# Kernel tuning notes

Measured on AMD Instinct MI355X. Metric: run time of the kernel, lower is better.

## Reference

```python
import jax, jax.numpy as jnp
import numpy as np

L, EMB, H, K, TASKS = 4, 256, 4, 3, 128
ATOM_VOCAB, BOND_VOCAB = 100, 10
N_NODES, N_EDGES, N_GRAPHS = 50000, 800000, 1024
FC_IN = EMB * (K + H + 1)  # 2048


def setup_inputs() -> dict:
    key = jax.random.key(0)
    ks = jax.random.split(key, 16)
    x = jax.random.randint(ks[0], (N_NODES, 9), 0, ATOM_VOCAB)
    edge_index = jax.random.randint(ks[1], (2, N_EDGES), 0, N_NODES)
    edge_attr = jax.random.randint(ks[2], (N_EDGES, 3), 0, BOND_VOCAB)
    batch = jnp.sort(jax.random.randint(ks[3], (N_NODES,), 0, N_GRAPHS))
    g = lambda k, shape, scale: jax.random.normal(k, shape, jnp.float32) * scale
    return {
        'x': x, 'edge_index': edge_index, 'edge_attr': edge_attr, 'batch': batch,
        'atom_emb': g(ks[4], (9, ATOM_VOCAB, EMB), 0.1),
        'bond_emb': g(ks[5], (L, 3, BOND_VOCAB, EMB), 0.1),
        'Wq_w': g(ks[6], (L, EMB, H * EMB), EMB ** -0.5),
        'Wq_b': jnp.zeros((L, H * EMB), jnp.float32),
        'Wk_w': g(ks[7], (L, EMB, H * EMB), EMB ** -0.5),
        'Wk_b': jnp.zeros((L, H * EMB), jnp.float32),
        'fc_w': g(ks[8], (L, FC_IN, EMB), FC_IN ** -0.5),
        'fc_b': jnp.zeros((L, EMB), jnp.float32),
        'ln_g': jnp.ones((L, EMB), jnp.float32),
        'ln_b': jnp.zeros((L, EMB), jnp.float32),
        'out_w': g(ks[9], (EMB, TASKS), EMB ** -0.5),
        'out_b': jnp.zeros((TASKS,), jnp.float32),
    }


def _layernorm(h, g, b, eps=1e-5):
    mu = h.mean(-1, keepdims=True)
    var = ((h - mu) ** 2).mean(-1, keepdims=True)
    return (h - mu) * jax.lax.rsqrt(var + eps) * g + b


def _linear_attn(h, wq, bq, wk, bk):
    # simple kernel, non-blockwise path of full_attention_conv
    N = h.shape[0]
    q = (h @ wq + bq).reshape(N, H, EMB)
    k = (h @ wk + bk).reshape(N, H, EMB)
    q = q / jnp.linalg.norm(q, axis=2, keepdims=True)
    k = k / jnp.linalg.norm(k, axis=2, keepdims=True)
    # value = x broadcast over heads -> contract with x directly
    kvs = jnp.einsum('lhm,ld->hmd', k, h)                 # [H,M,D]
    num = jnp.einsum('nhm,hmd->nhd', q, kvs) + h.sum(0)[None, None, :]
    ks_sum = k.sum(0)                                      # [H,M]
    denom = jnp.einsum('nhm,hm->nh', q, ks_sum)[..., None] + jnp.float32(N)
    return (num / denom).reshape(N, H * EMB)


def _gnn_high_order(h, row, col, e_emb):
    N = h.shape[0]
    ones = jnp.ones(row.shape[0], jnp.float32)
    deg_i = jax.ops.segment_sum(ones, row, num_segments=N)
    deg_j = jax.ops.segment_sum(ones, col, num_segments=N)
    dinv_i = jnp.where(deg_i > 0, deg_i ** -0.5, 0.0)
    dinv_j = jnp.where(deg_j > 0, deg_j ** -0.5, 0.0)
    adj_val = (dinv_i[row] * dinv_j[col])[:, None]         # [E,1]
    message = jax.ops.segment_sum(adj_val * e_emb, row, num_segments=N)
    xs = [h]
    for _ in range(K):
        spmm = jax.ops.segment_sum(adj_val * xs[-1][col], row, num_segments=N)
        xs.append(spmm + message)
    return jnp.concatenate(xs, axis=1)                     # [N, (K+1)*EMB]


def reference(x, edge_index, edge_attr, batch, atom_emb, bond_emb, Wq_w, Wq_b,
              Wk_w, Wk_b, fc_w, fc_b, ln_g, ln_b, out_w, out_b):
    row, col = edge_index[0], edge_index[1]
    # AtomEncoder: sum of 9 per-feature embeddings
    h = sum(atom_emb[f][x[:, f]] for f in range(9))        # [N, EMB]
    for i in range(L):
        x1 = _linear_attn(h, Wq_w[i], Wq_b[i], Wk_w[i], Wk_b[i])
        e_emb = sum(bond_emb[i, f][edge_attr[:, f]] for f in range(3))
        x2 = _gnn_high_order(h, row, col, e_emb)
        z = jnp.concatenate([x1, x2], axis=-1) @ fc_w[i] + fc_b[i]
        z = z + h  # residual
        z = _layernorm(z, ln_g[i], ln_b[i])
        h = jax.nn.relu(z)  # dropout = identity (eval)
    # mean pool per graph
    sums = jax.ops.segment_sum(h, batch, num_segments=N_GRAPHS)
    cnts = jax.ops.segment_sum(jnp.ones(h.shape[0], jnp.float32), batch, num_segments=N_GRAPHS)
    pooled = sums / jnp.maximum(cnts, 1.0)[:, None]
    return pooled @ out_w + out_b                           # [B, TASKS]
```

## Files before the change

### kernel.cpp

```cpp
#include <hip/hip_runtime.h>

#define DEV __device__ __forceinline__

constexpr int NN = 50000;
constexpr int NE = 800000;
constexpr int NG = 1024;
constexpr int EMB = 256;
constexpr int NH = 4;
constexpr int HE = 1024;
constexpr int NL = 4;
constexpr int TASKS = 128;
constexpr int NS = 50048;
constexpr int NCH = NS / 32;
constexpr int KVS_SL = 64;
constexpr int GB64 = NS / 64;
constexpr int GB128 = NS / 128;

using u16 = unsigned short;
using u32 = unsigned int;

typedef __attribute__((ext_vector_type(8))) short short8;
typedef __attribute__((ext_vector_type(4))) float f32x4;

#define MFMA16(a8, b8, c4) __builtin_amdgcn_mfma_f32_16x16x32_bf16(a8, b8, c4, 0, 0, 0)

DEV u16 f2bf(float f) {
  u32 u = __float_as_uint(f);
  u32 r = (u + 0x7FFFu + ((u >> 16) & 1u)) >> 16;
  return (u16)r;
}
DEV float bf2f(u16 s) { return __uint_as_float(((u32)s) << 16); }
DEV short8 ld8(const u16* p) { return *reinterpret_cast<const short8*>(p); }

DEV void gld16(const u16* g, u16* l) {
  __builtin_amdgcn_global_load_lds(
      (const __attribute__((address_space(1))) void*)g,
      (__attribute__((address_space(3))) void*)l, 16, 0, 0);
}

DEV void stage16_8(const u16* __restrict__ src, u16* dst, int w, int lane) {
#pragma unroll
  for (int i = 0; i < 2; ++i) {
    int f = w * 2 + i;
    gld16(src + (size_t)f * 512 + lane * 8, dst + f * 512);
  }
}

DEV void stage_rows128(const u16* __restrict__ src, u16* dst, int n0, int w, int lane) {
#pragma unroll
  for (int i = 0; i < 4; ++i) {
    int kc = w * 4 + i;
#pragma unroll
    for (int rh = 0; rh < 2; ++rh)
      gld16(src + (size_t)(n0 + rh * 64 + lane) * EMB + kc * 8,
            dst + (kc * 128 + rh * 64) * 8);
  }
}

DEV const u16* bsrc(int step, const u16* wqF, const u16* MTF, const u16* fcwF) {
  if (step > 95) step = 95;
  if (step < 64) {
    int hd = step >> 4, t = step & 15;
    if (t < 8) return wqF + ((size_t)(t * 64 + hd * 16)) * 512;
    return MTF + ((size_t)((t - 8) * 64 + hd * 16)) * 512;
  }
  return fcwF + ((size_t)(32 + (step - 64)) * 16) * 512;
}


__global__ void k_zero(u32* __restrict__ p, int n) {
  int i = blockIdx.x * 256 + threadIdx.x;
  if (i < n) p[i] = 0u;
}

__global__ void k_fill(float* __restrict__ p, int n, float v) {
  int i = blockIdx.x * 256 + threadIdx.x;
  if (i < n) p[i] = v;
}

__global__ void k_frag(const float* __restrict__ in, u16* __restrict__ outp,
                       int R, int rqTot, int rqStep, long inStride, long outStride) {
  int nc = blockIdx.x, rq = blockIdx.y, b = blockIdx.z;
  int l = threadIdx.x & 63;
  int g = l >> 4, s = l & 15;
  const float* ip = in + (size_t)b * inStride + (size_t)(nc * 32 + g * 8) * R + rq * 16 + s;
  short8 v;
#pragma unroll
  for (int j = 0; j < 8; ++j) v[j] = (short)f2bf(ip[(size_t)j * R]);
  u16* op = outp + (size_t)b * outStride +
            ((size_t)(nc * rqTot + b * rqStep + rq) * 64 + l) * 8;
  *reinterpret_cast<short8*>(op) = v;
}

__global__ void k_htrf(const u16* __restrict__ h_bf, u16* __restrict__ hF) {
  __shared__ u16 t[64][72];
  int tid = threadIdx.x;
  int n0 = blockIdx.x * 64, d0 = blockIdx.y * 64;
#pragma unroll
  for (int rr = 0; rr < 2; ++rr) {
    int nl = rr * 32 + (tid >> 3);
    int dd = (tid & 7) * 8;
    uint4 v = {0u, 0u, 0u, 0u};
    int n = n0 + nl;
    if (n < NN) v = *reinterpret_cast<const uint4*>(h_bf + (size_t)n * EMB + d0 + dd);
    *reinterpret_cast<uint4*>(&t[nl][dd]) = v;
  }
  __syncthreads();
#pragma unroll
  for (int k = 0; k < 2; ++k) {
    int u = tid + 256 * k;
    int nchL = u >> 8;
    int rqL = (u >> 6) & 3;
    int l = u & 63;
    int g = l >> 4, s = l & 15;
    short8 v;
#pragma unroll
    for (int j = 0; j < 8; ++j) v[j] = (short)t[nchL * 32 + g * 8 + j][rqL * 16 + s];
    *reinterpret_cast<short8*>(
        &hF[(((size_t)((n0 >> 5) + nchL) * 16 + (d0 >> 4) + rqL) * 64 + l) * 8]) = v;
  }
}


__global__ void k_atom(const int* __restrict__ x, const float* __restrict__ aemb,
                       u16* __restrict__ h_bf) {
  int n = blockIdx.x, d = threadIdx.x;
  const int* xr = x + n * 9;
  float acc = 0.f;
#pragma unroll
  for (int f = 0; f < 9; ++f) acc += aemb[(f * 100 + xr[f]) * EMB + d];
  h_bf[(size_t)n * EMB + d] = f2bf(acc);
}

__global__ void k_deg(const int* __restrict__ row, const int* __restrict__ col,
                      int* __restrict__ deg_i, int* __restrict__ deg_j) {
  int e = blockIdx.x * 256 + threadIdx.x;
  if (e < NE) {
    atomicAdd(&deg_i[row[e]], 1);
    atomicAdd(&deg_j[col[e]], 1);
  }
}

__global__ void k_dinv(const int* __restrict__ deg_i, const int* __restrict__ deg_j,
                       float* __restrict__ di, float* __restrict__ dj) {
  int n = blockIdx.x * 256 + threadIdx.x;
  if (n < NN) {
    di[n] = deg_i[n] > 0 ? rsqrtf((float)deg_i[n]) : 0.f;
    dj[n] = deg_j[n] > 0 ? rsqrtf((float)deg_j[n]) : 0.f;
  }
}

__global__ void k_scan(const int* __restrict__ deg, int* __restrict__ offs) {
  __shared__ int tot[1024];
  int t = threadIdx.x;
  constexpr int PER = (NN + 1023) / 1024;
  int lo = t * PER, hi = lo + PER;
  if (hi > NN) hi = NN;
  int s = 0;
  for (int i = lo; i < hi; ++i) s += deg[i];
  tot[t] = s;
  __syncthreads();
  for (int off = 1; off < 1024; off <<= 1) {
    int v = (t >= off) ? tot[t - off] : 0;
    __syncthreads();
    tot[t] += v;
    __syncthreads();
  }
  int run = (t == 0) ? 0 : tot[t - 1];
  for (int i = lo; i < hi; ++i) { offs[i] = run; run += deg[i]; }
  if (t == 0) offs[NN] = NE;
}

__global__ void k_csr(const int* __restrict__ row, const int* __restrict__ col,
                      const int* __restrict__ eattr, const float* __restrict__ di,
                      const float* __restrict__ dj, const int* __restrict__ offs,
                      int* __restrict__ cursor, int* __restrict__ csr_col,
                      float* __restrict__ csr_adj, int* __restrict__ csr_pack) {
  int e = blockIdx.x * 256 + threadIdx.x;
  if (e >= NE) return;
  int r = row[e], c = col[e];
  int slot = offs[r] + atomicAdd(&cursor[r], 1);
  csr_col[slot] = c;
  csr_adj[slot] = di[r] * dj[c];
  csr_pack[slot] = eattr[e * 3] | (eattr[e * 3 + 1] << 8) | (eattr[e * 3 + 2] << 16);
}

__global__ void k_gcnt(const int* __restrict__ batch, float* __restrict__ gcnt) {
  int n = blockIdx.x * 256 + threadIdx.x;
  if (n < NN) atomicAdd(&gcnt[batch[n]], 1.f);
}


__global__ void k_message(const float* __restrict__ bond, const int* __restrict__ offs,
                          const float* __restrict__ csr_adj, const int* __restrict__ csr_pack,
                          u16* __restrict__ msg) {
  __shared__ float tab[3 * 10 * EMB];
  int tid = threadIdx.x;
  for (int i = tid; i < 3 * 10 * EMB; i += 256) tab[i] = bond[i];
  __syncthreads();
  int n0 = blockIdx.x * 16;
  for (int nn = 0; nn < 16; ++nn) {
    int n = n0 + nn;
    int e0 = offs[n], e1 = offs[n + 1];
    float acc = 0.f;
    for (int s = e0; s < e1; ++s) {
      float a = csr_adj[s];
      int pk = csr_pack[s];
      int a0 = pk & 255, a1 = (pk >> 8) & 255, a2 = (pk >> 16) & 255;
      acc += a * (tab[a0 * EMB + tid] + tab[(10 + a1) * EMB + tid] + tab[(20 + a2) * EMB + tid]);
    }
    msg[(size_t)n * EMB + tid] = f2bf(acc);
  }
}

__global__ __launch_bounds__(256) void k_projk(
    const u16* __restrict__ h_bf, const u16* __restrict__ wkF, const float* __restrict__ bk,
    u16* __restrict__ knF, float* __restrict__ ks_sum, float* __restrict__ h_sum) {
  __shared__ __align__(16) u16 aL[32 * 64 * 8];
  __shared__ float red[4][EMB];
  int tid = threadIdx.x;
  int lane = tid & 63, w = tid >> 6;
  int g = lane >> 4, s = lane & 15;
  int n0 = blockIdx.x * 64;
  int hd = blockIdx.y;
  int wrow = w * 16;
  {
    int r = tid & 63, kq = tid >> 6;
#pragma unroll
    for (int ii = 0; ii < 8; ++ii) {
      int k = kq * 64 + ii * 8;
      int row = n0 + r;
      uint4 v = {0u, 0u, 0u, 0u};
      if (row < NN) v = *reinterpret_cast<const uint4*>(h_bf + (size_t)row * EMB + k);
      *reinterpret_cast<uint4*>(&aL[((k >> 3) * 64 + r) * 8]) = v;
    }
  }
  __syncthreads();
  if (hd == 0) {
    float ss = 0.f;
#pragma unroll 8
    for (int r = 0; r < 64; ++r) ss += bf2f(aL[((tid >> 3) * 64 + r) * 8 + (tid & 7)]);
    atomicAdd(&h_sum[tid], ss);
  }
  f32x4 ka[16] = {};
#pragma unroll
  for (int k0 = 0; k0 < 256; k0 += 32) {
    short8 a = ld8(&aL[(((k0 >> 3) + g) * 64 + wrow + s) * 8]);
#pragma unroll
    for (int c = 0; c < 16; ++c) {
      short8 b = ld8(&wkF[(((size_t)(k0 >> 5) * 64 + hd * 16 + c) * 64 + lane) * 8]);
      ka[c] = MFMA16(a, b, ka[c]);
    }
  }
  float nr[4] = {0.f, 0.f, 0.f, 0.f};
#pragma unroll
  for (int c = 0; c < 16; ++c) {
    float bv = bk[hd * 256 + c * 16 + s];
#pragma unroll
    for (int r = 0; r < 4; ++r) {
      ka[c][r] += bv;
      nr[r] += ka[c][r] * ka[c][r];
    }
  }
#pragma unroll
  for (int r = 0; r < 4; ++r) {
    nr[r] += __shfl_xor(nr[r], 1, 64);
    nr[r] += __shfl_xor(nr[r], 2, 64);
    nr[r] += __shfl_xor(nr[r], 4, 64);
    nr[r] += __shfl_xor(nr[r], 8, 64);
  }
  float rn[4];
#pragma unroll
  for (int r = 0; r < 4; ++r) {
    int row = n0 + wrow + g * 4 + r;
    rn[r] = (row < NN && nr[r] > 0.f) ? rsqrtf(nr[r]) : 0.f;
  }
  int nn = wrow + g * 4;
  int nch = (n0 + nn) >> 5;
  int gc = (nn >> 3) & 3;
  int jb = nn & 7;
  float cs[16];
#pragma unroll
  for (int c = 0; c < 16; ++c) {
    float v0 = ka[c][0] * rn[0], v1 = ka[c][1] * rn[1];
    float v2 = ka[c][2] * rn[2], v3 = ka[c][3] * rn[3];
    cs[c] = v0 + v1 + v2 + v3;
    ushort4 pk;
    pk.x = f2bf(v0); pk.y = f2bf(v1); pk.z = f2bf(v2); pk.w = f2bf(v3);
    *reinterpret_cast<ushort4*>(
        &knF[(((size_t)nch * 64 + hd * 16 + c) * 64 + gc * 16 + s) * 8 + jb]) = pk;
  }
#pragma unroll
  for (int c = 0; c < 16; ++c) {
    cs[c] += __shfl_xor(cs[c], 16, 64);
    cs[c] += __shfl_xor(cs[c], 32, 64);
  }
  if (g == 0) {
#pragma unroll
    for (int c = 0; c < 16; ++c) red[w][c * 16 + s] = cs[c];
  }
  __syncthreads();
  float tot = red[0][tid] + red[1][tid] + red[2][tid] + red[3][tid];
  atomicAdd(&ks_sum[hd * 256 + tid], tot);
}

__global__ __launch_bounds__(256) void k_kvs(const u16* __restrict__ knF,
                                             const u16* __restrict__ hF,
                                             float* __restrict__ kvs) {
  int tid = threadIdx.x;
  int lane = tid & 63, w = tid >> 6;
  int s = lane & 15, g = lane >> 4;
  int j0 = blockIdx.x * 128;
  int sl = blockIdx.y;
  f32x4 acc[8][4] = {};
  for (int ch = sl; ch < NCH; ch += KVS_SL) {
    short8 bfr[4];
#pragma unroll
    for (int df = 0; df < 4; ++df)
      bfr[df] = ld8(&hF[(((size_t)ch * 16 + w * 4 + df) * 64 + lane) * 8]);
#pragma unroll
    for (int jf = 0; jf < 8; ++jf) {
      short8 a = ld8(&knF[(((size_t)ch * 64 + (j0 >> 4) + jf) * 64 + lane) * 8]);
#pragma unroll
      for (int df = 0; df < 4; ++df) acc[jf][df] = MFMA16(a, bfr[df], acc[jf][df]);
    }
  }
#pragma unroll
  for (int jf = 0; jf < 8; ++jf)
#pragma unroll
    for (int df = 0; df < 4; ++df)
#pragma unroll
      for (int r = 0; r < 4; ++r)
        atomicAdd(&kvs[(size_t)(j0 + jf * 16 + g * 4 + r) * EMB + w * 64 + df * 16 + s],
                  acc[jf][df][r]);
}

__global__ void k_mpre(const float* __restrict__ kvs, const float* __restrict__ fcw,
                       float* __restrict__ M) {
  __shared__ float arow[EMB];
  int bid = blockIdx.x;
  int hd = bid >> 8;
  int t = threadIdx.x;
  arow[t] = kvs[(size_t)bid * EMB + t];
  __syncthreads();
  float acc = 0.f;
  const float* wp = fcw + (size_t)(hd * 256) * EMB + t;
#pragma unroll 4
  for (int d = 0; d < EMB; ++d) acc += arow[d] * wp[(size_t)d * EMB];
  M[(size_t)bid * EMB + t] = acc;
}

__global__ void k_cvec(const float* __restrict__ h_sum, const float* __restrict__ fcw,
                       float* __restrict__ c) {
  __shared__ float arow[EMB];
  int hd = blockIdx.x;
  int t = threadIdx.x;
  arow[t] = h_sum[t];
  __syncthreads();
  float acc = 0.f;
  const float* wp = fcw + (size_t)(hd * 256) * EMB + t;
#pragma unroll 4
  for (int d = 0; d < EMB; ++d) acc += arow[d] * wp[(size_t)d * EMB];
  c[hd * EMB + t] = acc;
}

__global__ __launch_bounds__(256) void k_spmm(
    const u16* __restrict__ xin, const u16* __restrict__ msg,
    const int* __restrict__ offs, const int* __restrict__ csr_col,
    const float* __restrict__ csr_adj, u16* __restrict__ sout) {
  int lane = threadIdx.x & 63, w = threadIdx.x >> 6;
  int n = blockIdx.x * 4 + w;
  if (n >= NN) return;
  int c4 = lane * 4;
  uint2 m = *reinterpret_cast<const uint2*>(msg + (size_t)n * EMB + c4);
  float a0 = bf2f(m.x & 0xffff), a1 = bf2f(m.x >> 16);
  float a2 = bf2f(m.y & 0xffff), a3 = bf2f(m.y >> 16);
  int e0 = offs[n], e1 = offs[n + 1];
  int s = e0;
  for (; s + 4 <= e1; s += 4) {
    int col0 = csr_col[s], col1 = csr_col[s + 1], col2 = csr_col[s + 2], col3 = csr_col[s + 3];
    float w0 = csr_adj[s], w1 = csr_adj[s + 1], w2 = csr_adj[s + 2], w3 = csr_adj[s + 3];
    uint2 r0 = *reinterpret_cast<const uint2*>(xin + (size_t)col0 * EMB + c4);
    uint2 r1 = *reinterpret_cast<const uint2*>(xin + (size_t)col1 * EMB + c4);
    uint2 r2 = *reinterpret_cast<const uint2*>(xin + (size_t)col2 * EMB + c4);
    uint2 r3 = *reinterpret_cast<const uint2*>(xin + (size_t)col3 * EMB + c4);
    a0 += w0 * bf2f(r0.x & 0xffff) + w1 * bf2f(r1.x & 0xffff) + w2 * bf2f(r2.x & 0xffff) + w3 * bf2f(r3.x & 0xffff);
    a1 += w0 * bf2f(r0.x >> 16)    + w1 * bf2f(r1.x >> 16)    + w2 * bf2f(r2.x >> 16)    + w3 * bf2f(r3.x >> 16);
    a2 += w0 * bf2f(r0.y & 0xffff) + w1 * bf2f(r1.y & 0xffff) + w2 * bf2f(r2.y & 0xffff) + w3 * bf2f(r3.y & 0xffff);
    a3 += w0 * bf2f(r0.y >> 16)    + w1 * bf2f(r1.y >> 16)    + w2 * bf2f(r2.y >> 16)    + w3 * bf2f(r3.y >> 16);
  }
  for (; s < e1; ++s) {
    int col = csr_col[s];
    float wv = csr_adj[s];
    uint2 r0 = *reinterpret_cast<const uint2*>(xin + (size_t)col * EMB + c4);
    a0 += wv * bf2f(r0.x & 0xffff);
    a1 += wv * bf2f(r0.x >> 16);
    a2 += wv * bf2f(r0.y & 0xffff);
    a3 += wv * bf2f(r0.y >> 16);
  }
  ushort4 o;
  o.x = f2bf(a0); o.y = f2bf(a1); o.z = f2bf(a2); o.w = f2bf(a3);
  *reinterpret_cast<ushort4*>(sout + (size_t)n * EMB + c4) = o;
}

__global__ __launch_bounds__(512) void k_fused(
    u16* __restrict__ h_bf,
    const u16* __restrict__ s1, const u16* __restrict__ s2, const u16* __restrict__ s3,
    const u16* __restrict__ wqF, const float* __restrict__ bq,
    const u16* __restrict__ MTF, const float* __restrict__ cvec, const float* __restrict__ kss,
    const u16* __restrict__ fcwF, const float* __restrict__ fcb,
    const float* __restrict__ lg, const float* __restrict__ lb) {
  __shared__ __align__(16) u16 aL[32 * 128 * 8];
  __shared__ __align__(16) u16 qL[16 * 128 * 8];
  __shared__ __align__(16) u16 bL[2][16 * 512];
  int tid = threadIdx.x;
  int lane = tid & 63, w = tid >> 6;
  int g = lane >> 4, s = lane & 15;
  int n0 = blockIdx.x * 128;
  int wrow = w * 16;

  stage_rows128(h_bf, aL, n0, w, lane);
  stage16_8(bsrc(0, wqF, MTF, fcwF), bL[0], w, lane);
  __syncthreads();

  f32x4 zac[16];
#pragma unroll
  for (int c = 0; c < 16; ++c) {
    int col = c * 16 + s;
#pragma unroll
    for (int r = 0; r < 4; ++r)
      zac[c][r] = bf2f(aL[((col >> 3) * 128 + wrow + g * 4 + r) * 8 + (col & 7)]);
  }

  int p = 0, step = 0;

  for (int hd = 0; hd < NH; ++hd) {
    f32x4 qa[16] = {};
#pragma unroll
    for (int kq = 0; kq < 8; ++kq) {
      stage16_8(bsrc(step + 1, wqF, MTF, fcwF), bL[p ^ 1], w, lane);
      short8 a = ld8(&aL[((kq * 4 + g) * 128 + wrow + s) * 8]);
#pragma unroll
      for (int c = 0; c < 16; ++c) {
        short8 b = ld8(&bL[p][c * 512 + lane * 8]);
        qa[c] = MFMA16(a, b, qa[c]);
      }
      __syncthreads();
      p ^= 1; ++step;
    }
    float nr[4] = {0.f, 0.f, 0.f, 0.f};
    float dp[4] = {0.f, 0.f, 0.f, 0.f};
#pragma unroll
    for (int c = 0; c < 16; ++c) {
      float bv = bq[hd * 256 + c * 16 + s];
      float kv = kss[hd * 256 + c * 16 + s];
#pragma unroll
      for (int r = 0; r < 4; ++r) {
        qa[c][r] += bv;
        nr[r] += qa[c][r] * qa[c][r];
        dp[r] += qa[c][r] * kv;
      }
    }
#pragma unroll
    for (int r = 0; r < 4; ++r) {
      nr[r] += __shfl_xor(nr[r], 1, 64);
      nr[r] += __shfl_xor(nr[r], 2, 64);
      nr[r] += __shfl_xor(nr[r], 4, 64);
      nr[r] += __shfl_xor(nr[r], 8, 64);
      dp[r] += __shfl_xor(dp[r], 1, 64);
      dp[r] += __shfl_xor(dp[r], 2, 64);
      dp[r] += __shfl_xor(dp[r], 4, 64);
      dp[r] += __shfl_xor(dp[r], 8, 64);
    }
    float sc[4], rdv[4];
#pragma unroll
    for (int r = 0; r < 4; ++r) {
      int row = n0 + wrow + g * 4 + r;
      float rn = (row < NN && nr[r] > 0.f) ? rsqrtf(nr[r]) : 0.f;
      rdv[r] = 1.f / (dp[r] * rn + (float)NN);
      sc[r] = rn * rdv[r];
    }
#pragma unroll
    for (int hh = 0; hh < 2; ++hh) {
#pragma unroll
      for (int c = hh * 8; c < hh * 8 + 8; ++c) {
        int mh = (c - hh * 8) * 16 + s;
#pragma unroll
        for (int r = 0; r < 4; ++r)
          qL[((mh >> 3) * 128 + wrow + g * 4 + r) * 8 + (mh & 7)] = f2bf(qa[c][r] * sc[r]);
      }
      __syncthreads();
#pragma unroll
      for (int k4 = 0; k4 < 4; ++k4) {
        stage16_8(bsrc(step + 1, wqF, MTF, fcwF), bL[p ^ 1], w, lane);
        short8 a = ld8(&qL[((k4 * 4 + g) * 128 + wrow + s) * 8]);
#pragma unroll
        for (int c = 0; c < 16; ++c) {
          short8 b = ld8(&bL[p][c * 512 + lane * 8]);
          zac[c] = MFMA16(a, b, zac[c]);
        }
        __syncthreads();
        p ^= 1; ++step;
      }
    }
#pragma unroll
    for (int c = 0; c < 16; ++c) {
      float cv = cvec[hd * 256 + c * 16 + s];
#pragma unroll
      for (int r = 0; r < 4; ++r) zac[c][r] += cv * rdv[r];
    }
  }

  for (int sg = 0; sg < 4; ++sg) {
    if (sg > 0) {
      const u16* sp = (sg == 1) ? s1 : (sg == 2) ? s2 : s3;
      stage_rows128(sp, aL, n0, w, lane);
      __syncthreads();
    }
#pragma unroll
    for (int kq = 0; kq < 8; ++kq) {
      stage16_8(bsrc(step + 1, wqF, MTF, fcwF), bL[p ^ 1], w, lane);
      short8 a = ld8(&aL[((kq * 4 + g) * 128 + wrow + s) * 8]);
#pragma unroll
      for (int c = 0; c < 16; ++c) {
        short8 b = ld8(&bL[p][c * 512 + lane * 8]);
        zac[c] = MFMA16(a, b, zac[c]);
      }
      __syncthreads();
      p ^= 1; ++step;
    }
  }

  float sm[4] = {0.f, 0.f, 0.f, 0.f}, sq[4] = {0.f, 0.f, 0.f, 0.f};
#pragma unroll
  for (int c = 0; c < 16; ++c) {
    int col = c * 16 + s;
    float fb = fcb[col];
#pragma unroll
    for (int r = 0; r < 4; ++r) {
      float v = zac[c][r] + fb;
      zac[c][r] = v;
      sm[r] += v;
      sq[r] += v * v;
    }
  }
#pragma unroll
  for (int r = 0; r < 4; ++r) {
    sm[r] += __shfl_xor(sm[r], 1, 64);
    sm[r] += __shfl_xor(sm[r], 2, 64);
    sm[r] += __shfl_xor(sm[r], 4, 64);
    sm[r] += __shfl_xor(sm[r], 8, 64);
    sq[r] += __shfl_xor(sq[r], 1, 64);
    sq[r] += __shfl_xor(sq[r], 2, 64);
    sq[r] += __shfl_xor(sq[r], 4, 64);
    sq[r] += __shfl_xor(sq[r], 8, 64);
  }
  float mu[4], rs[4];
#pragma unroll
  for (int r = 0; r < 4; ++r) {
    mu[r] = sm[r] * (1.f / 256.f);
    float var = sq[r] * (1.f / 256.f) - mu[r] * mu[r];
    rs[r] = rsqrtf(var + 1e-5f);
  }
#pragma unroll
  for (int c = 0; c < 16; ++c) {
    int col = c * 16 + s;
    float gg = lg[col], bb = lb[col];
#pragma unroll
    for (int r = 0; r < 4; ++r) {
      int row = n0 + wrow + g * 4 + r;
      if (row < NN) {
        float o = fmaxf(0.f, (zac[c][r] - mu[r]) * rs[r] * gg + bb);
        h_bf[(size_t)row * EMB + col] = f2bf(o);
      }
    }
  }
}


__global__ void k_pool(const u16* __restrict__ h_bf, const int* __restrict__ batch,
                       float* __restrict__ pooled) {
  int t = threadIdx.x;
  int n0 = blockIdx.x * 64;
  if (n0 >= NN) return;
  int nend = n0 + 64;
  if (nend > NN) nend = NN;
  float run = 0.f;
  int cur = batch[n0];
  for (int n = n0; n < nend; ++n) {
    int b = batch[n];
    if (b != cur) {
      atomicAdd(&pooled[(size_t)cur * EMB + t], run);
      run = 0.f;
      cur = b;
    }
    run += bf2f(h_bf[(size_t)n * EMB + t]);
  }
  atomicAdd(&pooled[(size_t)cur * EMB + t], run);
}

__global__ void k_out(const float* __restrict__ pooled, const float* __restrict__ gcnt,
                      const float* __restrict__ ow, const float* __restrict__ ob,
                      float* __restrict__ out) {
  __shared__ float prow[EMB];
  int g = blockIdx.x, t = threadIdx.x;
  float rc = 1.f / fmaxf(gcnt[g], 1.f);
  for (int i = t; i < EMB; i += TASKS) prow[i] = pooled[(size_t)g * EMB + i] * rc;
  __syncthreads();
  float acc = ob[t];
#pragma unroll 4
  for (int d = 0; d < EMB; ++d) acc += prow[d] * ow[d * TASKS + t];
  out[(size_t)g * TASKS + t] = acc;
}


extern "C" void kernel_launch(void* const* d_in, const int* in_sizes, int n_in,
                              void* d_out, int out_size, void* d_ws, size_t ws_size,
                              hipStream_t stream) {
  const int* x = (const int*)d_in[0];
  const int* eidx = (const int*)d_in[1];
  const int* eattr = (const int*)d_in[2];
  const int* batch = (const int*)d_in[3];
  const float* aemb = (const float*)d_in[4];
  const float* bemb = (const float*)d_in[5];
  const float* wq = (const float*)d_in[6];
  const float* bq = (const float*)d_in[7];
  const float* wk = (const float*)d_in[8];
  const float* bk = (const float*)d_in[9];
  const float* fcw = (const float*)d_in[10];
  const float* fcb = (const float*)d_in[11];
  const float* lg = (const float*)d_in[12];
  const float* lb = (const float*)d_in[13];
  const float* ow = (const float*)d_in[14];
  const float* ob = (const float*)d_in[15];
  float* out = (float*)d_out;

  size_t off = 0;
  auto alloc = [&](size_t bytes) -> void* {
    void* r = (char*)d_ws + off;
    off += (bytes + 255) & ~(size_t)255;
    return r;
  };
  u16* h_bf = (u16*)alloc((size_t)NN * EMB * 2);
  u16* region = (u16*)alloc((size_t)HE * NS * 2);
  u16* knF = region;
  u16* msg = region;
  u16* s1 = region + (size_t)NN * EMB;
  u16* s2 = region + (size_t)2 * NN * EMB;
  u16* s3 = region + (size_t)3 * NN * EMB;
  u16* hF = (u16*)alloc((size_t)EMB * NS * 2);
  float* kvs = (float*)alloc((size_t)HE * EMB * 4);
  float* Mm = (float*)alloc((size_t)HE * EMB * 4);
  u16* MTF = (u16*)alloc((size_t)HE * EMB * 2);
  u16* wqF = (u16*)alloc((size_t)NL * HE * EMB * 2);
  u16* wkF = (u16*)alloc((size_t)NL * HE * EMB * 2);
  u16* fcwF = (u16*)alloc((size_t)NL * 2048 * EMB * 2);
  float* cvec = (float*)alloc((size_t)NH * EMB * 4);
  float* ksh = (float*)alloc((size_t)(HE + EMB) * 4);
  float* ks_sum = ksh;
  float* h_sum = ksh + HE;
  float* dinv_i = (float*)alloc((size_t)NN * 4);
  float* dinv_j = (float*)alloc((size_t)NN * 4);
  int* deg_i = (int*)alloc((size_t)NN * 4);
  int* deg_j = (int*)alloc((size_t)NN * 4);
  int* offs = (int*)alloc((size_t)(NN + 1) * 4);
  int* cursor = (int*)alloc((size_t)NN * 4);
  int* csr_col = (int*)alloc((size_t)NE * 4);
  float* csr_adj = (float*)alloc((size_t)NE * 4);
  int* csr_pack = (int*)alloc((size_t)NE * 4);
  float* pooled = (float*)alloc((size_t)NG * EMB * 4);
  float* gcnt = (float*)alloc((size_t)NG * 4);

  if (off > ws_size) {
    k_fill<<<(out_size + 255) / 256, 256, 0, stream>>>(out, out_size, 1048576.f);
    return;
  }

  const int* row = eidx;
  const int* colp = eidx + NE;

  k_zero<<<(NN + 255) / 256, 256, 0, stream>>>((u32*)deg_i, NN);
  k_zero<<<(NN + 255) / 256, 256, 0, stream>>>((u32*)deg_j, NN);
  k_zero<<<(NN + 255) / 256, 256, 0, stream>>>((u32*)cursor, NN);
  k_zero<<<(NG + 255) / 256, 256, 0, stream>>>((u32*)gcnt, NG);
  k_zero<<<(NG * EMB + 255) / 256, 256, 0, stream>>>((u32*)pooled, NG * EMB);

  k_frag<<<dim3(8, 64, NL), 64, 0, stream>>>(wq, wqF, 1024, 64, 0,
                                             (long)EMB * HE, (long)HE * EMB);
  k_frag<<<dim3(8, 64, NL), 64, 0, stream>>>(wk, wkF, 1024, 64, 0,
                                             (long)EMB * HE, (long)HE * EMB);
  k_frag<<<dim3(64, 16, NL), 64, 0, stream>>>(fcw, fcwF, 256, 16, 0,
                                              (long)2048 * EMB, (long)2048 * EMB);

  k_atom<<<NN, EMB, 0, stream>>>(x, aemb, h_bf);
  k_deg<<<NE / 256, 256, 0, stream>>>(row, colp, deg_i, deg_j);
  k_dinv<<<(NN + 255) / 256, 256, 0, stream>>>(deg_i, deg_j, dinv_i, dinv_j);
  k_scan<<<1, 1024, 0, stream>>>(deg_i, offs);
  k_csr<<<NE / 256, 256, 0, stream>>>(row, colp, eattr, dinv_i, dinv_j, offs, cursor,
                                      csr_col, csr_adj, csr_pack);
  k_gcnt<<<(NN + 255) / 256, 256, 0, stream>>>(batch, gcnt);

  for (int l = 0; l < NL; ++l) {
    const float* fcw_l = fcw + (size_t)l * 2048 * EMB;
    k_zero<<<(HE + EMB + 255) / 256, 256, 0, stream>>>((u32*)ksh, HE + EMB);
    k_zero<<<(HE * EMB + 255) / 256, 256, 0, stream>>>((u32*)kvs, HE * EMB);
    k_projk<<<dim3(GB64, NH), 256, 0, stream>>>(h_bf, wkF + (size_t)l * HE * EMB,
                                                bk + (size_t)l * HE, knF, ks_sum, h_sum);
    k_htrf<<<dim3(GB64, 4), 256, 0, stream>>>(h_bf, hF);
    k_kvs<<<dim3(8, KVS_SL), 256, 0, stream>>>(knF, hF, kvs);
    k_mpre<<<HE, 256, 0, stream>>>(kvs, fcw_l, Mm);
    k_frag<<<dim3(8, 16, NH), 64, 0, stream>>>(Mm, MTF, 256, 64, 16,
                                               (long)EMB * EMB, 0);
    k_cvec<<<NH, 256, 0, stream>>>(h_sum, fcw_l, cvec);
    k_message<<<NN / 16, 256, 0, stream>>>(bemb + (size_t)l * 3 * 10 * EMB, offs, csr_adj,
                                           csr_pack, msg);
    k_spmm<<<NN / 4, 256, 0, stream>>>(h_bf, msg, offs, csr_col, csr_adj, s1);
    k_spmm<<<NN / 4, 256, 0, stream>>>(s1, msg, offs, csr_col, csr_adj, s2);
    k_spmm<<<NN / 4, 256, 0, stream>>>(s2, msg, offs, csr_col, csr_adj, s3);
    k_fused<<<GB128, 512, 0, stream>>>(h_bf, s1, s2, s3, wqF + (size_t)l * HE * EMB,
                                       bq + (size_t)l * HE, MTF, cvec, ks_sum,
                                       fcwF + (size_t)l * 2048 * EMB, fcb + (size_t)l * EMB,
                                       lg + (size_t)l * EMB, lb + (size_t)l * EMB);
  }
  k_pool<<<(NN + 63) / 64, 256, 0, stream>>>(h_bf, batch, pooled);
  k_out<<<NG, TASKS, 0, stream>>>(pooled, gcnt, ow, ob, out);
}
```

Measured before the change: 3.201 ms.

## Double B staging granularity in fused kernel, merge head loop in projk, widen kvs split

The fused kernel now stages two 16-fragment B tiles per pipeline step, halving the number of barriers and buffer swaps, with a larger LDS double buffer and a smaller q tile. k_projk loops over all four heads inside one block instead of one head per block, so the h tile is loaded into LDS once rather than four times. k_kvs is split across twice as many slices for more parallelism. The costs are more LDS per fused block, which may lower occupancy, fewer projk blocks with longer serial work, and more atomic contention in kvs.

```diff
diff --git a/kernel.cpp b/kernel.cpp
--- a/kernel.cpp
+++ b/kernel.cpp
@@ -12,7 +12,7 @@
 constexpr int TASKS = 128;
 constexpr int NS = 50048;
 constexpr int NCH = NS / 32;
-constexpr int KVS_SL = 64;
+constexpr int KVS_SL = 128;
 constexpr int GB64 = NS / 64;
 constexpr int GB128 = NS / 128;
 
@@ -36,14 +36,6 @@
   __builtin_amdgcn_global_load_lds(
       (const __attribute__((address_space(1))) void*)g,
       (__attribute__((address_space(3))) void*)l, 16, 0, 0);
-}
-
-DEV void stage16_8(const u16* __restrict__ src, u16* dst, int w, int lane) {
-#pragma unroll
-  for (int i = 0; i < 2; ++i) {
-    int f = w * 2 + i;
-    gld16(src + (size_t)f * 512 + lane * 8, dst + f * 512);
-  }
 }
 
 DEV void stage_rows128(const u16* __restrict__ src, u16* dst, int n0, int w, int lane) {
@@ -65,6 +57,18 @@
     return MTF + ((size_t)((t - 8) * 64 + hd * 16)) * 512;
   }
   return fcwF + ((size_t)(32 + (step - 64)) * 16) * 512;
+}
+
+DEV void stage_macro8(int m, const u16* wqF, const u16* MTF, const u16* fcwF,
+                      u16* dst, int w, int lane) {
+  const u16* sA = bsrc(2 * m, wqF, MTF, fcwF);
+  const u16* sB = bsrc(2 * m + 1, wqF, MTF, fcwF);
+#pragma unroll
+  for (int i = 0; i < 2; ++i) {
+    int f = w * 2 + i;
+    gld16(sA + (size_t)f * 512 + lane * 8, dst + f * 512);
+    gld16(sB + (size_t)f * 512 + lane * 8, dst + 8192 + f * 512);
+  }
 }
 
 
@@ -222,7 +226,6 @@
   int lane = tid & 63, w = tid >> 6;
   int g = lane >> 4, s = lane & 15;
   int n0 = blockIdx.x * 64;
-  int hd = blockIdx.y;
   int wrow = w * 16;
   {
     int r = tid & 63, kq = tid >> 6;
@@ -236,72 +239,75 @@
     }
   }
   __syncthreads();
-  if (hd == 0) {
+  {
     float ss = 0.f;
 #pragma unroll 8
     for (int r = 0; r < 64; ++r) ss += bf2f(aL[((tid >> 3) * 64 + r) * 8 + (tid & 7)]);
     atomicAdd(&h_sum[tid], ss);
   }
-  f32x4 ka[16] = {};
-#pragma unroll
-  for (int k0 = 0; k0 < 256; k0 += 32) {
-    short8 a = ld8(&aL[(((k0 >> 3) + g) * 64 + wrow + s) * 8]);
+  for (int hd = 0; hd < NH; ++hd) {
+    f32x4 ka[16] = {};
+#pragma unroll
+    for (int k0 = 0; k0 < 256; k0 += 32) {
+      short8 a = ld8(&aL[(((k0 >> 3) + g) * 64 + wrow + s) * 8]);
+#pragma unroll
+      for (int c = 0; c < 16; ++c) {
+        short8 b = ld8(&wkF[(((size_t)(k0 >> 5) * 64 + hd * 16 + c) * 64 + lane) * 8]);
+        ka[c] = MFMA16(a, b, ka[c]);
+      }
+    }
+    float nr[4] = {0.f, 0.f, 0.f, 0.f};
 #pragma unroll
     for (int c = 0; c < 16; ++c) {
-      short8 b = ld8(&wkF[(((size_t)(k0 >> 5) * 64 + hd * 16 + c) * 64 + lane) * 8]);
-      ka[c] = MFMA16(a, b, ka[c]);
-    }
-  }
-  float nr[4] = {0.f, 0.f, 0.f, 0.f};
-#pragma unroll
-  for (int c = 0; c < 16; ++c) {
-    float bv = bk[hd * 256 + c * 16 + s];
+      float bv = bk[hd * 256 + c * 16 + s];
+#pragma unroll
+      for (int r = 0; r < 4; ++r) {
+        ka[c][r] += bv;
+        nr[r] += ka[c][r] * ka[c][r];
+      }
+    }
 #pragma unroll
     for (int r = 0; r < 4; ++r) {
-      ka[c][r] += bv;
-      nr[r] += ka[c][r] * ka[c][r];
-    }
-  }
-#pragma unroll
-  for (int r = 0; r < 4; ++r) {
-    nr[r] += __shfl_xor(nr[r], 1, 64);
-    nr[r] += __shfl_xor(nr[r], 2, 64);
-    nr[r] += __shfl_xor(nr[r], 4, 64);
-    nr[r] += __shfl_xor(nr[r], 8, 64);
-  }
-  float rn[4];
-#pragma unroll
-  for (int r = 0; r < 4; ++r) {
-    int row = n0 + wrow + g * 4 + r;
-    rn[r] = (row < NN && nr[r] > 0.f) ? rsqrtf(nr[r]) : 0.f;
-  }
-  int nn = wrow + g * 4;
-  int nch = (n0 + nn) >> 5;
-  int gc = (nn >> 3) & 3;
-  int jb = nn & 7;
-  float cs[16];
-#pragma unroll
-  for (int c = 0; c < 16; ++c) {
-    float v0 = ka[c][0] * rn[0], v1 = ka[c][1] * rn[1];
-    float v2 = ka[c][2] * rn[2], v3 = ka[c][3] * rn[3];
-    cs[c] = v0 + v1 + v2 + v3;
-    ushort4 pk;
-    pk.x = f2bf(v0); pk.y = f2bf(v1); pk.z = f2bf(v2); pk.w = f2bf(v3);
-    *reinterpret_cast<ushort4*>(
-        &knF[(((size_t)nch * 64 + hd * 16 + c) * 64 + gc * 16 + s) * 8 + jb]) = pk;
-  }
-#pragma unroll
-  for (int c = 0; c < 16; ++c) {
-    cs[c] += __shfl_xor(cs[c], 16, 64);
-    cs[c] += __shfl_xor(cs[c], 32, 64);
-  }
-  if (g == 0) {
-#pragma unroll
-    for (int c = 0; c < 16; ++c) red[w][c * 16 + s] = cs[c];
-  }
-  __syncthreads();
-  float tot = red[0][tid] + red[1][tid] + red[2][tid] + red[3][tid];
-  atomicAdd(&ks_sum[hd * 256 + tid], tot);
+      nr[r] += __shfl_xor(nr[r], 1, 64);
+      nr[r] += __shfl_xor(nr[r], 2, 64);
+      nr[r] += __shfl_xor(nr[r], 4, 64);
+      nr[r] += __shfl_xor(nr[r], 8, 64);
+    }
+    float rn[4];
+#pragma unroll
+    for (int r = 0; r < 4; ++r) {
+      int row = n0 + wrow + g * 4 + r;
+      rn[r] = (row < NN && nr[r] > 0.f) ? rsqrtf(nr[r]) : 0.f;
+    }
+    int nn = wrow + g * 4;
+    int nch = (n0 + nn) >> 5;
+    int gc = (nn >> 3) & 3;
+    int jb = nn & 7;
+    float cs[16];
+#pragma unroll
+    for (int c = 0; c < 16; ++c) {
+      float v0 = ka[c][0] * rn[0], v1 = ka[c][1] * rn[1];
+      float v2 = ka[c][2] * rn[2], v3 = ka[c][3] * rn[3];
+      cs[c] = v0 + v1 + v2 + v3;
+      ushort4 pk;
+      pk.x = f2bf(v0); pk.y = f2bf(v1); pk.z = f2bf(v2); pk.w = f2bf(v3);
+      *reinterpret_cast<ushort4*>(
+          &knF[(((size_t)nch * 64 + hd * 16 + c) * 64 + gc * 16 + s) * 8 + jb]) = pk;
+    }
+#pragma unroll
+    for (int c = 0; c < 16; ++c) {
+      cs[c] += __shfl_xor(cs[c], 16, 64);
+      cs[c] += __shfl_xor(cs[c], 32, 64);
+    }
+    __syncthreads();
+    if (g == 0) {
+#pragma unroll
+      for (int c = 0; c < 16; ++c) red[w][c * 16 + s] = cs[c];
+    }
+    __syncthreads();
+    float tot = red[0][tid] + red[1][tid] + red[2][tid] + red[3][tid];
+    atomicAdd(&ks_sum[hd * 256 + tid], tot);
+  }
 }
 
 __global__ __launch_bounds__(256) void k_kvs(const u16* __restrict__ knF,
@@ -411,8 +417,8 @@
     const u16* __restrict__ fcwF, const float* __restrict__ fcb,
     const float* __restrict__ lg, const float* __restrict__ lb) {
   __shared__ __align__(16) u16 aL[32 * 128 * 8];
-  __shared__ __align__(16) u16 qL[16 * 128 * 8];
-  __shared__ __align__(16) u16 bL[2][16 * 512];
+  __shared__ __align__(16) u16 qL[8 * 128 * 8];
+  __shared__ __align__(16) u16 bL[2][2 * 8192];
   int tid = threadIdx.x;
   int lane = tid & 63, w = tid >> 6;
   int g = lane >> 4, s = lane & 15;
@@ -420,7 +426,7 @@
   int wrow = w * 16;
 
   stage_rows128(h_bf, aL, n0, w, lane);
-  stage16_8(bsrc(0, wqF, MTF, fcwF), bL[0], w, lane);
+  stage_macro8(0, wqF, MTF, fcwF, bL[0], w, lane);
   __syncthreads();
 
   f32x4 zac[16];
@@ -432,21 +438,25 @@
       zac[c][r] = bf2f(aL[((col >> 3) * 128 + wrow + g * 4 + r) * 8 + (col & 7)]);
   }
 
-  int p = 0, step = 0;
+  int p = 0, mstep = 0;
 
   for (int hd = 0; hd < NH; ++hd) {
     f32x4 qa[16] = {};
 #pragma unroll
-    for (int kq = 0; kq < 8; ++kq) {
-      stage16_8(bsrc(step + 1, wqF, MTF, fcwF), bL[p ^ 1], w, lane);
-      short8 a = ld8(&aL[((kq * 4 + g) * 128 + wrow + s) * 8]);
-#pragma unroll
-      for (int c = 0; c < 16; ++c) {
-        short8 b = ld8(&bL[p][c * 512 + lane * 8]);
-        qa[c] = MFMA16(a, b, qa[c]);
+    for (int mi = 0; mi < 4; ++mi) {
+      stage_macro8(mstep + 1, wqF, MTF, fcwF, bL[p ^ 1], w, lane);
+#pragma unroll
+      for (int sub = 0; sub < 2; ++sub) {
+        int kq = mi * 2 + sub;
+        short8 a = ld8(&aL[((kq * 4 + g) * 128 + wrow + s) * 8]);
+#pragma unroll
+        for (int c = 0; c < 16; ++c) {
+          short8 b = ld8(&bL[p][sub * 8192 + c * 512 + lane * 8]);
+          qa[c] = MFMA16(a, b, qa[c]);
+        }
       }
       __syncthreads();
-      p ^= 1; ++step;
+      p ^= 1; ++mstep;
     }
     float nr[4] = {0.f, 0.f, 0.f, 0.f};
     float dp[4] = {0.f, 0.f, 0.f, 0.f};
@@ -481,27 +491,27 @@
       sc[r] = rn * rdv[r];
     }
 #pragma unroll
-    for (int hh = 0; hh < 2; ++hh) {
-#pragma unroll
-      for (int c = hh * 8; c < hh * 8 + 8; ++c) {
-        int mh = (c - hh * 8) * 16 + s;
+    for (int qq = 0; qq < 4; ++qq) {
+#pragma unroll
+      for (int c = qq * 4; c < qq * 4 + 4; ++c) {
+        int mh = (c - qq * 4) * 16 + s;
 #pragma unroll
         for (int r = 0; r < 4; ++r)
           qL[((mh >> 3) * 128 + wrow + g * 4 + r) * 8 + (mh & 7)] = f2bf(qa[c][r] * sc[r]);
       }
       __syncthreads();
-#pragma unroll
-      for (int k4 = 0; k4 < 4; ++k4) {
-        stage16_8(bsrc(step + 1, wqF, MTF, fcwF), bL[p ^ 1], w, lane);
-        short8 a = ld8(&qL[((k4 * 4 + g) * 128 + wrow + s) * 8]);
+      stage_macro8(mstep + 1, wqF, MTF, fcwF, bL[p ^ 1], w, lane);
+#pragma unroll
+      for (int sub = 0; sub < 2; ++sub) {
+        short8 a = ld8(&qL[((sub * 4 + g) * 128 + wrow + s) * 8]);
 #pragma unroll
         for (int c = 0; c < 16; ++c) {
-          short8 b = ld8(&bL[p][c * 512 + lane * 8]);
+          short8 b = ld8(&bL[p][sub * 8192 + c * 512 + lane * 8]);
           zac[c] = MFMA16(a, b, zac[c]);
         }
-        __syncthreads();
-        p ^= 1; ++step;
       }
+      __syncthreads();
+      p ^= 1; ++mstep;
     }
 #pragma unroll
     for (int c = 0; c < 16; ++c) {
@@ -518,16 +528,20 @@
       __syncthreads();
     }
 #pragma unroll
-    for (int kq = 0; kq < 8; ++kq) {
-      stage16_8(bsrc(step + 1, wqF, MTF, fcwF), bL[p ^ 1], w, lane);
-      short8 a = ld8(&aL[((kq * 4 + g) * 128 + wrow + s) * 8]);
-#pragma unroll
-      for (int c = 0; c < 16; ++c) {
-        short8 b = ld8(&bL[p][c * 512 + lane * 8]);
-        zac[c] = MFMA16(a, b, zac[c]);
+    for (int mi = 0; mi < 4; ++mi) {
+      stage_macro8(mstep + 1, wqF, MTF, fcwF, bL[p ^ 1], w, lane);
+#pragma unroll
+      for (int sub = 0; sub < 2; ++sub) {
+        int kq = mi * 2 + sub;
+        short8 a = ld8(&aL[((kq * 4 + g) * 128 + wrow + s) * 8]);
+#pragma unroll
+        for (int c = 0; c < 16; ++c) {
+          short8 b = ld8(&bL[p][sub * 8192 + c * 512 + lane * 8]);
+          zac[c] = MFMA16(a, b, zac[c]);
+        }
       }
       __syncthreads();
-      p ^= 1; ++step;
+      p ^= 1; ++mstep;
     }
   }
 
@@ -704,8 +718,8 @@
     const float* fcw_l = fcw + (size_t)l * 2048 * EMB;
     k_zero<<<(HE + EMB + 255) / 256, 256, 0, stream>>>((u32*)ksh, HE + EMB);
     k_zero<<<(HE * EMB + 255) / 256, 256, 0, stream>>>((u32*)kvs, HE * EMB);
-    k_projk<<<dim3(GB64, NH), 256, 0, stream>>>(h_bf, wkF + (size_t)l * HE * EMB,
-                                                bk + (size_t)l * HE, knF, ks_sum, h_sum);
+    k_projk<<<GB64, 256, 0, stream>>>(h_bf, wkF + (size_t)l * HE * EMB,
+                                      bk + (size_t)l * HE, knF, ks_sum, h_sum);
     k_htrf<<<dim3(GB64, 4), 256, 0, stream>>>(h_bf, hF);
     k_kvs<<<dim3(8, KVS_SL), 256, 0, stream>>>(knF, hF, kvs);
     k_mpre<<<HE, 256, 0, stream>>>(kvs, fcw_l, Mm);
```

Measured after the change: 4.082 ms, median of 3. +27.5%, slower.
